# Kernel tuning notes

Measured on AMD Instinct MI355X. Metric: run time of the kernel, lower is better.

Reference implementation:

```python
import jax, jax.numpy as jnp
import numpy as np

B, N, E, H = 2, 64, 128, 8
D = E // H
LN_EPS = 1e-5


def setup_inputs() -> dict:
    key = jax.random.key(0)
    ks = jax.random.split(key, 20)
    s = 1.0 / np.sqrt(E)
    sa = 1.0 / np.sqrt(E // 2)
    f32 = jnp.float32
    return {
        "pair_emb": jax.random.normal(ks[0], (B, N, N, E), f32),
        "tri_emb": jax.random.normal(ks[1], (B, N, N, N, E // 2), f32),
        "pair_mask": jnp.ones((B, N, N, 1), f32),
        "ln_g": jnp.ones((E,), f32),
        "ln_b": jnp.zeros((E,), f32),
        "Wq": jax.random.normal(ks[2], (E, E), f32) * s,
        "bq": jnp.zeros((E,), f32),
        "Wke": jax.random.normal(ks[3], (E, E), f32) * s,
        "bke": jnp.zeros((E,), f32),
        "Wka": jax.random.normal(ks[4], (E // 2, E), f32) * sa,
        "bka": jnp.zeros((E,), f32),
        "Wv": jax.random.normal(ks[5], (E, E), f32) * s,
        "bv": jnp.zeros((E,), f32),
        "Wva": jax.random.normal(ks[6], (E // 2, E), f32) * sa,
        "bva": jnp.zeros((E,), f32),
        "Wo": jax.random.normal(ks[7], (E, E), f32) * s,
        "bo": jnp.zeros((E,), f32),
        "Wg": jax.random.normal(ks[8], (E, E), f32) * s,
        "bg": jnp.zeros((E,), f32),
        "batch_size": B,
        "n_nodes": N,
    }


def reference(pair_emb, tri_emb, pair_mask, ln_g, ln_b, Wq, bq, Wke, bke,
              Wka, bka, Wv, bv, Wva, bva, Wo, bo, Wg, bg,
              batch_size, n_nodes):
    b, n = batch_size, n_nodes
    # bias[b,x,j] = (1 - pair_mask[b,j,x,0]) * 1e-9  (faithful to source, incl. 1e-9)
    bias = (1.0 - jnp.transpose(pair_mask[..., 0], (0, 2, 1))) * 1e-9
    pe = pair_emb - jnp.mean(pair_emb, axis=-1, keepdims=True)
    pe = pe * jax.lax.rsqrt(jnp.var(pair_emb, axis=-1, keepdims=True) + LN_EPS)
    pe = pe * ln_g + ln_b  # LayerNorm(pair_emb)
    scale = 1.0 / np.sqrt(D)
    # q[b,i,x,h,d]
    q = ((pe @ Wq + bq) * scale).reshape(b, n, n, H, D)
    # k_e[b,i,j,h,d] broadcast over x; k_a[b,i,x,j,h,d]
    k_e = (pe @ Wke + bke).reshape(b, n, n, H, D)
    k_a = (tri_emb @ Wka + bka).reshape(b, n, n, n, H, D)
    k = k_e[:, :, None] + k_a  # [b,i,x,j,h,d]
    # scores[b,i,x,h,j] ; softmax over j (last key axis)
    scores = jnp.einsum('bixhd,bixjhd->bixhj', q, k) + bias[:, None, :, None, :]
    attn = jax.nn.softmax(scores, axis=-1)  # attn_dropout is identity in eval
    v_e = (pe @ Wv + bv).reshape(b, n, n, H, D)
    v_a = (tri_emb @ Wva + bva).reshape(b, n, n, n, H, D)
    v = v_e[:, :, None] + v_a  # [b,i,x,j,h,d]
    out = jnp.einsum('bixhj,bixjhd->bixhd', attn, v).reshape(b, n, n, E)
    out = out @ Wo + bo
    gate = jax.nn.sigmoid(pe @ Wg + bg)
    return out * gate
```

## Files before the change

kernel.cpp:

```cpp
#include <hip/hip_runtime.h>

#define NB 2
#define NN 64
#define NE 128
#define NH 8
#define ND 16
#define NC 64
#define NROWS (NB*NN*NN)

__global__ __launch_bounds__(256) void tri_k1(
    const float* __restrict__ pair_emb,
    const float* __restrict__ ln_g, const float* __restrict__ ln_b,
    const float* __restrict__ Wq, const float* __restrict__ bq,
    const float* __restrict__ Wke, const float* __restrict__ bke,
    const float* __restrict__ Wv, const float* __restrict__ bv,
    const float* __restrict__ Wg, const float* __restrict__ bg,
    float* __restrict__ qo, float* __restrict__ keo,
    float* __restrict__ veo, float* __restrict__ gateo)
{
    __shared__ float pe_s[16][NE];
    const int tid = threadIdx.x;
    const int wave = tid >> 6, lane = tid & 63;
    const int row0 = blockIdx.x * 16;

    for (int r = wave * 4; r < wave * 4 + 4; ++r) {
        const int row = row0 + r;
        float2 v = *reinterpret_cast<const float2*>(&pair_emb[(size_t)row * NE + lane * 2]);
        float s = v.x + v.y, s2 = v.x * v.x + v.y * v.y;
        #pragma unroll
        for (int m = 1; m < 64; m <<= 1) { s += __shfl_xor(s, m); s2 += __shfl_xor(s2, m); }
        const float mean = s * (1.0f / NE);
        const float var = fmaxf(s2 * (1.0f / NE) - mean * mean, 0.0f);
        const float inv = rsqrtf(var + 1e-5f);
        pe_s[r][lane * 2]     = (v.x - mean) * inv * ln_g[lane * 2]     + ln_b[lane * 2];
        pe_s[r][lane * 2 + 1] = (v.y - mean) * inv * ln_g[lane * 2 + 1] + ln_b[lane * 2 + 1];
    }
    __syncthreads();

    const int o = tid & 127;
    const int half = tid >> 7;
    float aq[8] = {0,0,0,0,0,0,0,0}, ak[8] = {0,0,0,0,0,0,0,0};
    float av[8] = {0,0,0,0,0,0,0,0}, ag[8] = {0,0,0,0,0,0,0,0};
    for (int c = 0; c < NE; ++c) {
        const float wq = Wq[c * NE + o];
        const float wk = Wke[c * NE + o];
        const float wv = Wv[c * NE + o];
        const float wg = Wg[c * NE + o];
        #pragma unroll
        for (int r = 0; r < 8; ++r) {
            const float p = pe_s[half * 8 + r][c];
            aq[r] += p * wq; ak[r] += p * wk; av[r] += p * wv; ag[r] += p * wg;
        }
    }
    #pragma unroll
    for (int r = 0; r < 8; ++r) {
        const size_t row = (size_t)row0 + half * 8 + r;
        qo[row * NE + o]    = (aq[r] + bq[o]) * 0.25f;
        keo[row * NE + o]   = ak[r] + bke[o];
        veo[row * NE + o]   = av[r] + bv[o];
        gateo[row * NE + o] = 1.0f / (1.0f + __expf(-(ag[r] + bg[o])));
    }
}

__global__ __launch_bounds__(256) void tri_k1b(
    const float* __restrict__ qv, const float* __restrict__ kev,
    const float* __restrict__ mask,
    const float* __restrict__ Wka, const float* __restrict__ bka,
    float* __restrict__ S0g, float* __restrict__ qwg)
{
    __shared__ float qt[NN][129];
    __shared__ float ket[NN][NE];
    __shared__ float wka_s[NC][NE];
    __shared__ float msk[NN][NN];
    __shared__ float bka_s[NE];

    const int tid = threadIdx.x;
    const int blk = blockIdx.x;
    const int b = blk >> 6;
    const size_t base = (size_t)blk * NN;

    #pragma unroll
    for (int k = 0; k < 8; ++k) {
        const int v = tid + k * 256;
        const int r = v >> 5, c4 = (v & 31) * 4;
        float4 t = *reinterpret_cast<const float4*>(&qv[(base + r) * NE + c4]);
        qt[r][c4 + 0] = t.x; qt[r][c4 + 1] = t.y; qt[r][c4 + 2] = t.z; qt[r][c4 + 3] = t.w;
        *reinterpret_cast<float4*>(&ket[r][c4]) =
            *reinterpret_cast<const float4*>(&kev[(base + r) * NE + c4]);
        *reinterpret_cast<float4*>(&wka_s[r][c4]) =
            *reinterpret_cast<const float4*>(&Wka[(size_t)r * NE + c4]);
    }
    #pragma unroll
    for (int k = 0; k < 4; ++k) {
        const int v = tid + k * 256;
        const int j = v >> 4, x4 = (v & 15) * 4;
        *reinterpret_cast<float4*>(&msk[j][x4]) =
            *reinterpret_cast<const float4*>(&mask[(size_t)b * 4096 + j * 64 + x4]);
    }
    if (tid < 32) {
        *reinterpret_cast<float4*>(&bka_s[tid * 4]) =
            *reinterpret_cast<const float4*>(&bka[tid * 4]);
    }
    __syncthreads();

    const int x2 = tid & 31, h = tid >> 5;
    const int xA = x2, xB = x2 + 32;
    float qA[16], qB[16];
    #pragma unroll
    for (int d = 0; d < 16; ++d) { qA[d] = qt[xA][h * 16 + d]; qB[d] = qt[xB][h * 16 + d]; }
    float qbA = 0.0f, qbB = 0.0f;
    #pragma unroll
    for (int d = 0; d < 16; ++d) { const float bk = bka_s[h * 16 + d]; qbA += qA[d] * bk; qbB += qB[d] * bk; }

    for (int j4 = 0; j4 < 16; ++j4) {
        float sA[4], sB[4];
        #pragma unroll
        for (int jj = 0; jj < 4; ++jj) {
            const int j = j4 * 4 + jj;
            float aA = qbA + 1e-9f * (1.0f - msk[j][xA]);
            float aB = qbB + 1e-9f * (1.0f - msk[j][xB]);
            const float4* kj = reinterpret_cast<const float4*>(&ket[j][h * 16]);
            #pragma unroll
            for (int d4 = 0; d4 < 4; ++d4) {
                const float4 kv = kj[d4];
                aA += qA[d4*4+0]*kv.x + qA[d4*4+1]*kv.y + qA[d4*4+2]*kv.z + qA[d4*4+3]*kv.w;
                aB += qB[d4*4+0]*kv.x + qB[d4*4+1]*kv.y + qB[d4*4+2]*kv.z + qB[d4*4+3]*kv.w;
            }
            sA[jj] = aA; sB[jj] = aB;
        }
        *reinterpret_cast<float4*>(&S0g[(base + xA) * 512 + h * 64 + j4 * 4]) =
            make_float4(sA[0], sA[1], sA[2], sA[3]);
        *reinterpret_cast<float4*>(&S0g[(base + xB) * 512 + h * 64 + j4 * 4]) =
            make_float4(sB[0], sB[1], sB[2], sB[3]);
    }
    for (int c4 = 0; c4 < 16; ++c4) {
        float sA[4], sB[4];
        #pragma unroll
        for (int cc = 0; cc < 4; ++cc) {
            const int c = c4 * 4 + cc;
            float aA = 0.0f, aB = 0.0f;
            const float4* wj = reinterpret_cast<const float4*>(&wka_s[c][h * 16]);
            #pragma unroll
            for (int d4 = 0; d4 < 4; ++d4) {
                const float4 wv = wj[d4];
                aA += qA[d4*4+0]*wv.x + qA[d4*4+1]*wv.y + qA[d4*4+2]*wv.z + qA[d4*4+3]*wv.w;
                aB += qB[d4*4+0]*wv.x + qB[d4*4+1]*wv.y + qB[d4*4+2]*wv.z + qB[d4*4+3]*wv.w;
            }
            sA[cc] = aA; sB[cc] = aB;
        }
        *reinterpret_cast<float4*>(&qwg[(base + xA) * 512 + h * 64 + c4 * 4]) =
            make_float4(sA[0], sA[1], sA[2], sA[3]);
        *reinterpret_cast<float4*>(&qwg[(base + xB) * 512 + h * 64 + c4 * 4]) =
            make_float4(sB[0], sB[1], sB[2], sB[3]);
    }
}

__global__ __launch_bounds__(256) void tri_k2(
    const float* __restrict__ tri, const float* __restrict__ S0g,
    const float* __restrict__ qwg, const float* __restrict__ vev,
    float* __restrict__ tg, float* __restrict__ preg)
{
    __shared__ float tri_s[64][68];
    __shared__ float qw_s[8][68];
    __shared__ float sc_s[8][72];
    __shared__ float pre_p[2][128];

    const int tid = threadIdx.x;
    const int bix = blockIdx.x;
    const int base_bi = bix & ~63;

    const float4* tri4 = reinterpret_cast<const float4*>(tri) + (size_t)bix * 1024;
    #pragma unroll
    for (int k = 0; k < 4; ++k) {
        const int v = tid + k * 256;
        const int j = v >> 4, c4 = (v & 15) * 4;
        *reinterpret_cast<float4*>(&tri_s[j][c4]) = tri4[v];
    }
    {
        const int i0 = tid, i1 = tid + 256;
        qw_s[i0 >> 6][i0 & 63] = qwg[(size_t)bix * 512 + i0];
        qw_s[i1 >> 6][i1 & 63] = qwg[(size_t)bix * 512 + i1];
        sc_s[i0 >> 6][i0 & 63] = S0g[(size_t)bix * 512 + i0];
        sc_s[i1 >> 6][i1 & 63] = S0g[(size_t)bix * 512 + i1];
    }
    __syncthreads();

    {
        const int h = tid & 7, j0 = tid >> 3;
        float a0 = sc_s[h][j0], a1 = sc_s[h][j0 + 32];
        #pragma unroll 4
        for (int c4 = 0; c4 < 64; c4 += 4) {
            const float4 w  = *reinterpret_cast<const float4*>(&qw_s[h][c4]);
            const float4 t0 = *reinterpret_cast<const float4*>(&tri_s[j0][c4]);
            const float4 t1 = *reinterpret_cast<const float4*>(&tri_s[j0 + 32][c4]);
            a0 += t0.x * w.x + t0.y * w.y + t0.z * w.z + t0.w * w.w;
            a1 += t1.x * w.x + t1.y * w.y + t1.z * w.z + t1.w * w.w;
        }
        sc_s[h][j0] = a0;
        sc_s[h][j0 + 32] = a1;
    }
    __syncthreads();

    {
        const int hh = tid >> 5, l = tid & 31;
        const float v0 = sc_s[hh][l], v1 = sc_s[hh][l + 32];
        float m = fmaxf(v0, v1);
        #pragma unroll
        for (int msk = 1; msk < 32; msk <<= 1) m = fmaxf(m, __shfl_xor(m, msk));
        const float e0 = __expf(v0 - m), e1 = __expf(v1 - m);
        float s = e0 + e1;
        #pragma unroll
        for (int msk = 1; msk < 32; msk <<= 1) s += __shfl_xor(s, msk);
        const float inv = 1.0f / s;
        sc_s[hh][l] = e0 * inv;
        sc_s[hh][l + 32] = e1 * inv;
    }
    __syncthreads();

    {
        const int c = tid & 63, h2 = tid >> 6;
        float acc0 = 0.0f, acc1 = 0.0f;
        #pragma unroll 8
        for (int j = 0; j < 64; ++j) {
            const float tv = tri_s[j][c];
            acc0 += sc_s[h2][j] * tv;
            acc1 += sc_s[h2 + 4][j] * tv;
        }
        tg[(size_t)bix * 512 + tid]       = acc0;
        tg[(size_t)bix * 512 + tid + 256] = acc1;
    }
    {
        const int e = tid & 127, g = tid >> 7;
        const int hh = e >> 4;
        float acc = 0.0f;
        #pragma unroll 4
        for (int j = g * 32; j < g * 32 + 32; ++j)
            acc += sc_s[hh][j] * vev[(size_t)(base_bi + j) * NE + e];
        pre_p[g][e] = acc;
    }
    __syncthreads();
    if (tid < 128) preg[(size_t)bix * NE + tid] = pre_p[0][tid] + pre_p[1][tid];
}

__global__ __launch_bounds__(256) void tri_k3(
    const float* __restrict__ tg, const float* __restrict__ preg,
    const float* __restrict__ gatev,
    const float* __restrict__ Wva, const float* __restrict__ bva,
    const float* __restrict__ Wo, const float* __restrict__ bo,
    float* __restrict__ out)
{
    __shared__ float wva_s[64][160];
    __shared__ float wo_s[128][128];
    __shared__ float o_s[32][132];

    const int tid = threadIdx.x;
    const int row0 = blockIdx.x * 32;

    #pragma unroll
    for (int k = 0; k < 8; ++k) {
        const int v = tid + k * 256;
        const int c = v >> 5, e4 = (v & 31) * 4;
        const int col = e4 + ((e4 >> 4) << 2);
        *reinterpret_cast<float4*>(&wva_s[c][col]) =
            *reinterpret_cast<const float4*>(&Wva[(size_t)c * NE + e4]);
    }
    #pragma unroll
    for (int k = 0; k < 16; ++k) {
        const int v = tid + k * 256;
        const int kk = v >> 5, e4 = (v & 31) * 4;
        *reinterpret_cast<float4*>(&wo_s[kk][e4]) =
            *reinterpret_cast<const float4*>(&Wo[(size_t)kk * NE + e4]);
    }
    __syncthreads();

    {
        const int r = tid >> 3, h = tid & 7;
        const size_t row = (size_t)row0 + r;
        float4 acc[4];
        #pragma unroll
        for (int d4 = 0; d4 < 4; ++d4) {
            const float4 p  = *reinterpret_cast<const float4*>(&preg[row * NE + h * 16 + d4 * 4]);
            const float4 bv = *reinterpret_cast<const float4*>(&bva[h * 16 + d4 * 4]);
            acc[d4].x = p.x + bv.x; acc[d4].y = p.y + bv.y;
            acc[d4].z = p.z + bv.z; acc[d4].w = p.w + bv.w;
        }
        const float4* tp = reinterpret_cast<const float4*>(&tg[row * 512 + h * 64]);
        for (int c4 = 0; c4 < 16; ++c4) {
            const float4 tv = tp[c4];
            const float tc[4] = {tv.x, tv.y, tv.z, tv.w};
            #pragma unroll
            for (int cc = 0; cc < 4; ++cc) {
                const int c = c4 * 4 + cc;
                const float t0 = tc[cc];
                #pragma unroll
                for (int d4 = 0; d4 < 4; ++d4) {
                    const float4 w = *reinterpret_cast<const float4*>(&wva_s[c][20 * h + d4 * 4]);
                    acc[d4].x += t0 * w.x; acc[d4].y += t0 * w.y;
                    acc[d4].z += t0 * w.z; acc[d4].w += t0 * w.w;
                }
            }
        }
        #pragma unroll
        for (int d4 = 0; d4 < 4; ++d4)
            *reinterpret_cast<float4*>(&o_s[r][h * 16 + d4 * 4]) = acc[d4];
    }
    __syncthreads();

    {
        const int e4 = (tid & 31) * 4, rg = tid >> 5;
        const float4 b4 = *reinterpret_cast<const float4*>(&bo[e4]);
        float4 acc[4];
        #pragma unroll
        for (int rr = 0; rr < 4; ++rr) acc[rr] = b4;
        #pragma unroll 4
        for (int k = 0; k < 128; ++k) {
            const float4 w = *reinterpret_cast<const float4*>(&wo_s[k][e4]);
            #pragma unroll
            for (int rr = 0; rr < 4; ++rr) {
                const float ov = o_s[rg * 4 + rr][k];
                acc[rr].x += ov * w.x; acc[rr].y += ov * w.y;
                acc[rr].z += ov * w.z; acc[rr].w += ov * w.w;
            }
        }
        #pragma unroll
        for (int rr = 0; rr < 4; ++rr) {
            const size_t row = (size_t)row0 + rg * 4 + rr;
            const float4 g = *reinterpret_cast<const float4*>(&gatev[row * NE + e4]);
            float4 o;
            o.x = acc[rr].x * g.x; o.y = acc[rr].y * g.y;
            o.z = acc[rr].z * g.z; o.w = acc[rr].w * g.w;
            *reinterpret_cast<float4*>(&out[row * NE + e4]) = o;
        }
    }
}

extern "C" void kernel_launch(void* const* d_in, const int* in_sizes, int n_in,
                              void* d_out, int out_size, void* d_ws, size_t ws_size,
                              hipStream_t stream)
{
    const float* pair_emb = (const float*)d_in[0];
    const float* tri_emb  = (const float*)d_in[1];
    const float* mask     = (const float*)d_in[2];
    const float* ln_g = (const float*)d_in[3];
    const float* ln_b = (const float*)d_in[4];
    const float* Wq  = (const float*)d_in[5];  const float* bq  = (const float*)d_in[6];
    const float* Wke = (const float*)d_in[7];  const float* bke = (const float*)d_in[8];
    const float* Wka = (const float*)d_in[9];  const float* bka = (const float*)d_in[10];
    const float* Wv  = (const float*)d_in[11]; const float* bv  = (const float*)d_in[12];
    const float* Wva = (const float*)d_in[13]; const float* bva = (const float*)d_in[14];
    const float* Wo  = (const float*)d_in[15]; const float* bo  = (const float*)d_in[16];
    const float* Wg  = (const float*)d_in[17]; const float* bg  = (const float*)d_in[18];

    float* ws = (float*)d_ws;
    float* qo    = ws;
    float* keo   = qo    + (size_t)NROWS * NE;
    float* veo   = keo   + (size_t)NROWS * NE;
    float* gateo = veo   + (size_t)NROWS * NE;
    float* qwg   = gateo + (size_t)NROWS * NE;
    float* S0g   = qwg   + (size_t)NROWS * 512;
    float* tg    = S0g   + (size_t)NROWS * 512;
    float* preg  = tg    + (size_t)NROWS * 512;

    hipLaunchKernelGGL(tri_k1, dim3(NROWS / 16), dim3(256), 0, stream,
        pair_emb, ln_g, ln_b, Wq, bq, Wke, bke, Wv, bv, Wg, bg,
        qo, keo, veo, gateo);
    hipLaunchKernelGGL(tri_k1b, dim3(NB * NN), dim3(256), 0, stream,
        qo, keo, mask, Wka, bka, S0g, qwg);
    hipLaunchKernelGGL(tri_k2, dim3(NROWS), dim3(256), 0, stream,
        tri_emb, S0g, qwg, veo, tg, preg);
    hipLaunchKernelGGL(tri_k3, dim3(NROWS / 32), dim3(256), 0, stream,
        tg, preg, gateo, Wva, bva, Wo, bo, (float*)d_out);
}
```

Baseline: 148.5 us.

## Pipeline tri_k2 over 8 x-rows with register prefetch and shared v_e tile

tri_k2 now has each block handle 8 consecutive x rows for one (b,i). It stages the v_e tile in shared memory once and prefetches the next row's tri/qw/S0 data into registers while computing the current row, using double-buffered shared arrays. Blocks are remapped so each XCD handles a contiguous group of (b,i). tri_k1b is split into two blocks per (b,i), each covering half the x range, to double its parallelism. This removes repeated global reads of v_e, hides load latency, and adds register and LDS pressure, which may reduce occupancy.

```diff
diff --git a/kernel.cpp b/kernel.cpp
--- a/kernel.cpp
+++ b/kernel.cpp
@@ -68,23 +68,23 @@
     const float* __restrict__ Wka, const float* __restrict__ bka,
     float* __restrict__ S0g, float* __restrict__ qwg)
 {
-    __shared__ float qt[NN][129];
+    __shared__ float qt[32][129];
     __shared__ float ket[NN][NE];
     __shared__ float wka_s[NC][NE];
-    __shared__ float msk[NN][NN];
+    __shared__ float msk[NN][33];
     __shared__ float bka_s[NE];
 
     const int tid = threadIdx.x;
-    const int blk = blockIdx.x;
+    const int blk = blockIdx.x >> 1;
+    const int xh  = blockIdx.x & 1;
     const int b = blk >> 6;
     const size_t base = (size_t)blk * NN;
+    const int xloc0 = xh * 32;
 
     #pragma unroll
     for (int k = 0; k < 8; ++k) {
         const int v = tid + k * 256;
         const int r = v >> 5, c4 = (v & 31) * 4;
-        float4 t = *reinterpret_cast<const float4*>(&qv[(base + r) * NE + c4]);
-        qt[r][c4 + 0] = t.x; qt[r][c4 + 1] = t.y; qt[r][c4 + 2] = t.z; qt[r][c4 + 3] = t.w;
         *reinterpret_cast<float4*>(&ket[r][c4]) =
             *reinterpret_cast<const float4*>(&kev[(base + r) * NE + c4]);
         *reinterpret_cast<float4*>(&wka_s[r][c4]) =
@@ -93,9 +93,15 @@
     #pragma unroll
     for (int k = 0; k < 4; ++k) {
         const int v = tid + k * 256;
-        const int j = v >> 4, x4 = (v & 15) * 4;
-        *reinterpret_cast<float4*>(&msk[j][x4]) =
-            *reinterpret_cast<const float4*>(&mask[(size_t)b * 4096 + j * 64 + x4]);
+        const int r = v >> 5, c4 = (v & 31) * 4;
+        float4 tq = *reinterpret_cast<const float4*>(&qv[(base + xloc0 + r) * NE + c4]);
+        qt[r][c4] = tq.x; qt[r][c4+1] = tq.y; qt[r][c4+2] = tq.z; qt[r][c4+3] = tq.w;
+    }
+    #pragma unroll
+    for (int k = 0; k < 8; ++k) {
+        const int v = tid + k * 256;
+        const int j = v >> 5, xl = v & 31;
+        msk[j][xl] = mask[(size_t)b * 4096 + j * 64 + xloc0 + xl];
     }
     if (tid < 32) {
         *reinterpret_cast<float4*>(&bka_s[tid * 4]) =
@@ -103,55 +109,48 @@
     }
     __syncthreads();
 
-    const int x2 = tid & 31, h = tid >> 5;
-    const int xA = x2, xB = x2 + 32;
-    float qA[16], qB[16];
-    #pragma unroll
-    for (int d = 0; d < 16; ++d) { qA[d] = qt[xA][h * 16 + d]; qB[d] = qt[xB][h * 16 + d]; }
-    float qbA = 0.0f, qbB = 0.0f;
-    #pragma unroll
-    for (int d = 0; d < 16; ++d) { const float bk = bka_s[h * 16 + d]; qbA += qA[d] * bk; qbB += qB[d] * bk; }
+    const int xl = tid & 31, h = tid >> 5;
+    const int x = xloc0 + xl;
+    float qA[16];
+    #pragma unroll
+    for (int d = 0; d < 16; ++d) qA[d] = qt[xl][h * 16 + d];
+    float qbA = 0.0f;
+    #pragma unroll
+    for (int d = 0; d < 16; ++d) qbA += qA[d] * bka_s[h * 16 + d];
 
     for (int j4 = 0; j4 < 16; ++j4) {
-        float sA[4], sB[4];
+        float sA[4];
         #pragma unroll
         for (int jj = 0; jj < 4; ++jj) {
             const int j = j4 * 4 + jj;
-            float aA = qbA + 1e-9f * (1.0f - msk[j][xA]);
-            float aB = qbB + 1e-9f * (1.0f - msk[j][xB]);
+            float aA = qbA + 1e-9f * (1.0f - msk[j][xl]);
             const float4* kj = reinterpret_cast<const float4*>(&ket[j][h * 16]);
             #pragma unroll
             for (int d4 = 0; d4 < 4; ++d4) {
                 const float4 kv = kj[d4];
                 aA += qA[d4*4+0]*kv.x + qA[d4*4+1]*kv.y + qA[d4*4+2]*kv.z + qA[d4*4+3]*kv.w;
-                aB += qB[d4*4+0]*kv.x + qB[d4*4+1]*kv.y + qB[d4*4+2]*kv.z + qB[d4*4+3]*kv.w;
-            }
-            sA[jj] = aA; sB[jj] = aB;
-        }
-        *reinterpret_cast<float4*>(&S0g[(base + xA) * 512 + h * 64 + j4 * 4]) =
+            }
+            sA[jj] = aA;
+        }
+        *reinterpret_cast<float4*>(&S0g[(base + x) * 512 + h * 64 + j4 * 4]) =
             make_float4(sA[0], sA[1], sA[2], sA[3]);
-        *reinterpret_cast<float4*>(&S0g[(base + xB) * 512 + h * 64 + j4 * 4]) =
-            make_float4(sB[0], sB[1], sB[2], sB[3]);
     }
     for (int c4 = 0; c4 < 16; ++c4) {
-        float sA[4], sB[4];
+        float sA[4];
         #pragma unroll
         for (int cc = 0; cc < 4; ++cc) {
             const int c = c4 * 4 + cc;
-            float aA = 0.0f, aB = 0.0f;
+            float aA = 0.0f;
             const float4* wj = reinterpret_cast<const float4*>(&wka_s[c][h * 16]);
             #pragma unroll
             for (int d4 = 0; d4 < 4; ++d4) {
                 const float4 wv = wj[d4];
                 aA += qA[d4*4+0]*wv.x + qA[d4*4+1]*wv.y + qA[d4*4+2]*wv.z + qA[d4*4+3]*wv.w;
-                aB += qB[d4*4+0]*wv.x + qB[d4*4+1]*wv.y + qB[d4*4+2]*wv.z + qB[d4*4+3]*wv.w;
-            }
-            sA[cc] = aA; sB[cc] = aB;
-        }
-        *reinterpret_cast<float4*>(&qwg[(base + xA) * 512 + h * 64 + c4 * 4]) =
+            }
+            sA[cc] = aA;
+        }
+        *reinterpret_cast<float4*>(&qwg[(base + x) * 512 + h * 64 + c4 * 4]) =
             make_float4(sA[0], sA[1], sA[2], sA[3]);
-        *reinterpret_cast<float4*>(&qwg[(base + xB) * 512 + h * 64 + c4 * 4]) =
-            make_float4(sB[0], sB[1], sB[2], sB[3]);
     }
 }
 
@@ -160,86 +159,121 @@
     const float* __restrict__ qwg, const float* __restrict__ vev,
     float* __restrict__ tg, float* __restrict__ preg)
 {
-    __shared__ float tri_s[64][68];
-    __shared__ float qw_s[8][68];
-    __shared__ float sc_s[8][72];
+    __shared__ float vev_s[64][128];
+    __shared__ float tri_s[2][64][68];
+    __shared__ float qw_s[2][8][68];
+    __shared__ float sc_s[2][8][72];
     __shared__ float pre_p[2][128];
 
     const int tid = threadIdx.x;
-    const int bix = blockIdx.x;
-    const int base_bi = bix & ~63;
-
-    const float4* tri4 = reinterpret_cast<const float4*>(tri) + (size_t)bix * 1024;
-    #pragma unroll
-    for (int k = 0; k < 4; ++k) {
-        const int v = tid + k * 256;
-        const int j = v >> 4, c4 = (v & 15) * 4;
-        *reinterpret_cast<float4*>(&tri_s[j][c4]) = tri4[v];
-    }
+    const int bid = blockIdx.x;
+    const int xcd = bid & 7, slot = bid >> 3;
+    const int g = slot >> 4;
+    const int bi = xcd * 16 + (slot & 15);
+    const size_t base_bi = (size_t)bi * NN;
+    const int x0 = g * 8;
+
+    #pragma unroll
+    for (int k = 0; k < 8; ++k) {
+        const int v = tid + k * 256;
+        const int j = v >> 5, e4 = (v & 31) * 4;
+        *reinterpret_cast<float4*>(&vev_s[j][e4]) =
+            *reinterpret_cast<const float4*>(&vev[(base_bi + j) * NE + e4]);
+    }
+
+    float4 pf0, pf1, pf2, pf3;
+    float pqw0, pqw1, ps0, ps1;
     {
-        const int i0 = tid, i1 = tid + 256;
-        qw_s[i0 >> 6][i0 & 63] = qwg[(size_t)bix * 512 + i0];
-        qw_s[i1 >> 6][i1 & 63] = qwg[(size_t)bix * 512 + i1];
-        sc_s[i0 >> 6][i0 & 63] = S0g[(size_t)bix * 512 + i0];
-        sc_s[i1 >> 6][i1 & 63] = S0g[(size_t)bix * 512 + i1];
-    }
-    __syncthreads();
-
-    {
-        const int h = tid & 7, j0 = tid >> 3;
-        float a0 = sc_s[h][j0], a1 = sc_s[h][j0 + 32];
-        #pragma unroll 4
-        for (int c4 = 0; c4 < 64; c4 += 4) {
-            const float4 w  = *reinterpret_cast<const float4*>(&qw_s[h][c4]);
-            const float4 t0 = *reinterpret_cast<const float4*>(&tri_s[j0][c4]);
-            const float4 t1 = *reinterpret_cast<const float4*>(&tri_s[j0 + 32][c4]);
-            a0 += t0.x * w.x + t0.y * w.y + t0.z * w.z + t0.w * w.w;
-            a1 += t1.x * w.x + t1.y * w.y + t1.z * w.z + t1.w * w.w;
-        }
-        sc_s[h][j0] = a0;
-        sc_s[h][j0 + 32] = a1;
-    }
-    __syncthreads();
-
-    {
-        const int hh = tid >> 5, l = tid & 31;
-        const float v0 = sc_s[hh][l], v1 = sc_s[hh][l + 32];
-        float m = fmaxf(v0, v1);
-        #pragma unroll
-        for (int msk = 1; msk < 32; msk <<= 1) m = fmaxf(m, __shfl_xor(m, msk));
-        const float e0 = __expf(v0 - m), e1 = __expf(v1 - m);
-        float s = e0 + e1;
-        #pragma unroll
-        for (int msk = 1; msk < 32; msk <<= 1) s += __shfl_xor(s, msk);
-        const float inv = 1.0f / s;
-        sc_s[hh][l] = e0 * inv;
-        sc_s[hh][l + 32] = e1 * inv;
-    }
-    __syncthreads();
-
-    {
-        const int c = tid & 63, h2 = tid >> 6;
-        float acc0 = 0.0f, acc1 = 0.0f;
-        #pragma unroll 8
-        for (int j = 0; j < 64; ++j) {
-            const float tv = tri_s[j][c];
-            acc0 += sc_s[h2][j] * tv;
-            acc1 += sc_s[h2 + 4][j] * tv;
-        }
-        tg[(size_t)bix * 512 + tid]       = acc0;
-        tg[(size_t)bix * 512 + tid + 256] = acc1;
-    }
-    {
-        const int e = tid & 127, g = tid >> 7;
-        const int hh = e >> 4;
-        float acc = 0.0f;
-        #pragma unroll 4
-        for (int j = g * 32; j < g * 32 + 32; ++j)
-            acc += sc_s[hh][j] * vev[(size_t)(base_bi + j) * NE + e];
-        pre_p[g][e] = acc;
-    }
-    __syncthreads();
-    if (tid < 128) preg[(size_t)bix * NE + tid] = pre_p[0][tid] + pre_p[1][tid];
+        const float4* tp = reinterpret_cast<const float4*>(tri) + (base_bi + x0) * 1024;
+        pf0 = tp[tid]; pf1 = tp[tid + 256]; pf2 = tp[tid + 512]; pf3 = tp[tid + 768];
+        const size_t q0 = (base_bi + x0) * 512;
+        pqw0 = qwg[q0 + tid]; pqw1 = qwg[q0 + tid + 256];
+        ps0  = S0g[q0 + tid]; ps1  = S0g[q0 + tid + 256];
+    }
+
+    int cur = 0;
+    for (int t = 0; t < 8; ++t) {
+        {
+            const int jw = tid >> 4, c4w = (tid & 15) * 4;
+            *reinterpret_cast<float4*>(&tri_s[cur][jw][c4w])      = pf0;
+            *reinterpret_cast<float4*>(&tri_s[cur][jw + 16][c4w]) = pf1;
+            *reinterpret_cast<float4*>(&tri_s[cur][jw + 32][c4w]) = pf2;
+            *reinterpret_cast<float4*>(&tri_s[cur][jw + 48][c4w]) = pf3;
+            qw_s[cur][tid >> 6][tid & 63]       = pqw0;
+            qw_s[cur][(tid >> 6) + 4][tid & 63] = pqw1;
+            sc_s[cur][tid >> 6][tid & 63]       = ps0;
+            sc_s[cur][(tid >> 6) + 4][tid & 63] = ps1;
+        }
+        __syncthreads();
+
+        if (t < 7) {
+            const int x = x0 + t + 1;
+            const float4* tp = reinterpret_cast<const float4*>(tri) + (base_bi + x) * 1024;
+            pf0 = tp[tid]; pf1 = tp[tid + 256]; pf2 = tp[tid + 512]; pf3 = tp[tid + 768];
+            const size_t q0 = (base_bi + x) * 512;
+            pqw0 = qwg[q0 + tid]; pqw1 = qwg[q0 + tid + 256];
+            ps0  = S0g[q0 + tid]; ps1  = S0g[q0 + tid + 256];
+        }
+
+        {
+            const int h = tid & 7, j0 = tid >> 3;
+            float a0 = sc_s[cur][h][j0], a1 = sc_s[cur][h][j0 + 32];
+            #pragma unroll 4
+            for (int c4 = 0; c4 < 64; c4 += 4) {
+                const float4 w  = *reinterpret_cast<const float4*>(&qw_s[cur][h][c4]);
+                const float4 t0 = *reinterpret_cast<const float4*>(&tri_s[cur][j0][c4]);
+                const float4 t1 = *reinterpret_cast<const float4*>(&tri_s[cur][j0 + 32][c4]);
+                a0 += t0.x * w.x + t0.y * w.y + t0.z * w.z + t0.w * w.w;
+                a1 += t1.x * w.x + t1.y * w.y + t1.z * w.z + t1.w * w.w;
+            }
+            sc_s[cur][h][j0] = a0;
+            sc_s[cur][h][j0 + 32] = a1;
+        }
+        __syncthreads();
+
+        {
+            const int hh = tid >> 5, l = tid & 31;
+            const float v0 = sc_s[cur][hh][l], v1 = sc_s[cur][hh][l + 32];
+            float m = fmaxf(v0, v1);
+            #pragma unroll
+            for (int msk = 1; msk < 32; msk <<= 1) m = fmaxf(m, __shfl_xor(m, msk));
+            const float e0 = __expf(v0 - m), e1 = __expf(v1 - m);
+            float s = e0 + e1;
+            #pragma unroll
+            for (int msk = 1; msk < 32; msk <<= 1) s += __shfl_xor(s, msk);
+            const float inv = 1.0f / s;
+            sc_s[cur][hh][l] = e0 * inv;
+            sc_s[cur][hh][l + 32] = e1 * inv;
+        }
+        __syncthreads();
+
+        const size_t bix = base_bi + x0 + t;
+        {
+            const int c = tid & 63, h2 = tid >> 6;
+            float acc0 = 0.0f, acc1 = 0.0f;
+            #pragma unroll 8
+            for (int j = 0; j < 64; ++j) {
+                const float tv = tri_s[cur][j][c];
+                acc0 += sc_s[cur][h2][j] * tv;
+                acc1 += sc_s[cur][h2 + 4][j] * tv;
+            }
+            tg[bix * 512 + tid]       = acc0;
+            tg[bix * 512 + tid + 256] = acc1;
+        }
+        {
+            const int e = tid & 127, g2 = tid >> 7;
+            const int hh = e >> 4;
+            float acc = 0.0f;
+            #pragma unroll 8
+            for (int j = g2 * 32; j < g2 * 32 + 32; ++j)
+                acc += sc_s[cur][hh][j] * vev_s[j][e];
+            pre_p[g2][e] = acc;
+        }
+        __syncthreads();
+        if (tid < 128)
+            preg[bix * NE + tid] = pre_p[0][tid] + pre_p[1][tid];
+        cur ^= 1;
+    }
 }
 
 __global__ __launch_bounds__(256) void tri_k3(
@@ -325,10 +359,10 @@
         #pragma unroll
         for (int rr = 0; rr < 4; ++rr) {
             const size_t row = (size_t)row0 + rg * 4 + rr;
-            const float4 g = *reinterpret_cast<const float4*>(&gatev[row * NE + e4]);
+            const float4 gt = *reinterpret_cast<const float4*>(&gatev[row * NE + e4]);
             float4 o;
-            o.x = acc[rr].x * g.x; o.y = acc[rr].y * g.y;
-            o.z = acc[rr].z * g.z; o.w = acc[rr].w * g.w;
+            o.x = acc[rr].x * gt.x; o.y = acc[rr].y * gt.y;
+            o.z = acc[rr].z * gt.z; o.w = acc[rr].w * gt.w;
             *reinterpret_cast<float4*>(&out[row * NE + e4]) = o;
         }
     }
@@ -364,9 +398,9 @@
     hipLaunchKernelGGL(tri_k1, dim3(NROWS / 16), dim3(256), 0, stream,
         pair_emb, ln_g, ln_b, Wq, bq, Wke, bke, Wv, bv, Wg, bg,
         qo, keo, veo, gateo);
-    hipLaunchKernelGGL(tri_k1b, dim3(NB * NN), dim3(256), 0, stream,
+    hipLaunchKernelGGL(tri_k1b, dim3(NB * NN * 2), dim3(256), 0, stream,
         qo, keo, mask, Wka, bka, S0g, qwg);
-    hipLaunchKernelGGL(tri_k2, dim3(NROWS), dim3(256), 0, stream,
+    hipLaunchKernelGGL(tri_k2, dim3(NROWS / 8), dim3(256), 0, stream,
         tri_emb, S0g, qwg, veo, tg, preg);
     hipLaunchKernelGGL(tri_k3, dim3(NROWS / 32), dim3(256), 0, stream,
         tg, preg, gateo, Wva, bva, Wo, bo, (float*)d_out);
```

Result: slower. 155.0 us (+4.4%).
